# Performance work log

Hardware: AMD Instinct MI355X
Metric: run time of the kernel (lower is better)

## Reference

```python
import jax, jax.numpy as jnp
import numpy as np

D_MODEL = 1024
NUM_HEADS = 16
D_K = D_MODEL // NUM_HEADS


def setup_inputs() -> dict:
    key = jax.random.key(0)
    ks = jax.random.split(key, 8)
    s = 1.0 / np.sqrt(D_MODEL)
    inp = {
        'q': jax.random.normal(ks[0], (2, 2048, D_MODEL), jnp.float32),
        'k': jax.random.normal(ks[1], (2, 2048, D_MODEL), jnp.float32),
        'v': jax.random.normal(ks[2], (2, 2048, D_MODEL), jnp.float32),
        'Wq': jax.random.normal(ks[3], (D_MODEL, D_MODEL), jnp.float32) * s,
        'bq': jnp.zeros((D_MODEL,), jnp.float32),
        'Wk': jax.random.normal(ks[4], (D_MODEL, D_MODEL), jnp.float32) * s,
        'bk': jnp.zeros((D_MODEL,), jnp.float32),
        'Wv': jax.random.normal(ks[5], (D_MODEL, D_MODEL), jnp.float32) * s,
        'bv': jnp.zeros((D_MODEL,), jnp.float32),
        'Wo': jax.random.normal(ks[6], (D_MODEL, D_MODEL), jnp.float32) * s,
        'bo': jnp.zeros((D_MODEL,), jnp.float32),
    }
    return inp


def _split_heads(x):
    # [B, S, D] -> [B, H, S, d_k]
    b, s, _ = x.shape
    return x.reshape(b, s, NUM_HEADS, D_K).transpose(0, 2, 1, 3)


def reference(q, k, v, Wq, bq, Wk, bk, Wv, bv, Wo, bo):
    qh = _split_heads(q @ Wq + bq)
    kh = _split_heads(k @ Wk + bk)
    vh = _split_heads(v @ Wv + bv)
    scale = 1.0 / jnp.sqrt(jnp.asarray(D_K, qh.dtype))
    scores = jnp.einsum('bhqd,bhkd->bhqk', qh, kh) * scale  # [B,H,S,S]
    probs = jax.nn.softmax(scores, axis=-1)
    ctx = jnp.einsum('bhqk,bhkd->bhqd', probs, vh)
    b, h, s, d = ctx.shape
    ctx = ctx.transpose(0, 2, 1, 3).reshape(b, s, h * d)
    return ctx @ Wo + bo
```

## Files before the change

kernel.cpp:

```cpp
#include <hip/hip_runtime.h>

#define D_MODEL 1024
#define SEQ     2048
#define BATCH   2
#define NH      16
#define DK      64
#define MROWS   (BATCH*SEQ)

typedef __attribute__((ext_vector_type(8))) short short8;
typedef __attribute__((ext_vector_type(4))) float f32x4;
typedef __attribute__((ext_vector_type(16))) float f32x16;

#define QSCALE 0.18033688011112042f

#if __has_builtin(__builtin_amdgcn_exp2f)
#define EXP2(x) __builtin_amdgcn_exp2f(x)
#else
#define EXP2(x) exp2f(x)
#endif

static __device__ __forceinline__ unsigned short f2bf(float f) {
  unsigned u = __float_as_uint(f);
  u += 0x7fff + ((u >> 16) & 1);
  return (unsigned short)(u >> 16);
}

static __device__ __forceinline__ unsigned pack_bf2(float a, float b) {
  unsigned ua = __float_as_uint(a) + 0x8000u;
  unsigned ub = __float_as_uint(b) + 0x8000u;
#if __has_builtin(__builtin_amdgcn_perm)
  return __builtin_amdgcn_perm(ub, ua, 0x07060302u);
#else
  return (ua >> 16) | (ub & 0xffff0000u);
#endif
}

static __device__ __forceinline__ void plswap(unsigned& x, unsigned& y, int h) {
#if __has_builtin(__builtin_amdgcn_permlane32_swap)
  typedef __attribute__((ext_vector_type(2))) unsigned uint2v;
  uint2v r = __builtin_amdgcn_permlane32_swap(x, y, false, false);
  x = r.x; y = r.y;
#else
  unsigned xs = __shfl_xor((int)x, 32), ys = __shfl_xor((int)y, 32);
  unsigned nx = h ? ys : x;
  unsigned ny = h ? y : xs;
  x = nx; y = ny;
#endif
}

static __device__ __forceinline__ void load16_lds(const void* g, void* l) {
  __builtin_amdgcn_global_load_lds(
      (const __attribute__((address_space(1))) void*)g,
      (__attribute__((address_space(3))) void*)l, 16, 0, 0);
}

__global__ void cvt_all(const float* __restrict__ q, const float* __restrict__ k,
                        const float* __restrict__ v, unsigned short* __restrict__ out, int n4) {
  int i = blockIdx.x * blockDim.x + threadIdx.x;
  if (i >= n4) return;
  const float* src = (blockIdx.y == 0) ? q : (blockIdx.y == 1) ? k : v;
  float4 val = ((const float4*)src)[i];
  unsigned r0 = (unsigned)f2bf(val.x) | ((unsigned)f2bf(val.y) << 16);
  unsigned r1 = (unsigned)f2bf(val.z) | ((unsigned)f2bf(val.w) << 16);
  uint2 u; u.x = r0; u.y = r1;
  ((uint2*)(out + (size_t)blockIdx.y * MROWS * D_MODEL))[i] = u;
}

__global__ void wtrans_all(const float* __restrict__ Wq, const float* __restrict__ Wk,
                           const float* __restrict__ Wv, const float* __restrict__ Wo,
                           unsigned short* __restrict__ Wt) {
  __shared__ float t[32][33];
  const float* W = (blockIdx.z == 0) ? Wq : (blockIdx.z == 1) ? Wk
                 : (blockIdx.z == 2) ? Wv : Wo;
  unsigned short* dst = Wt + (size_t)blockIdx.z * D_MODEL * D_MODEL;
  int n0 = blockIdx.x * 32, k0 = blockIdx.y * 32;
  int tx = threadIdx.x & 31, ty = threadIdx.x >> 5;
#pragma unroll
  for (int i = 0; i < 32; i += 8)
    t[ty + i][tx] = W[(size_t)(k0 + ty + i) * D_MODEL + n0 + tx];
  __syncthreads();
#pragma unroll
  for (int i = 0; i < 32; i += 8)
    dst[(size_t)(n0 + ty + i) * D_MODEL + k0 + tx] = f2bf(t[tx][ty + i]);
}

__global__ __launch_bounds__(256, 2) void gemm_qkv(
    const unsigned short* __restrict__ Abig,
    const unsigned short* __restrict__ Wt,
    const float* __restrict__ bq, const float* __restrict__ bk, const float* __restrict__ bv,
    unsigned short* __restrict__ Qh, unsigned short* __restrict__ Kh,
    unsigned short* __restrict__ Vt)
{
  constexpr int K = D_MODEL;
  __shared__ unsigned short As[128 * 32];
  __shared__ unsigned short Bs[128 * 32];
  const int g = blockIdx.y >> 5;
  const unsigned short* A  = Abig + (size_t)g * MROWS * K;
  const unsigned short* Bt = Wt + (size_t)g * K * K;
  const float* bias = (g == 0) ? bq : (g == 1) ? bk : bv;
  unsigned short* out = (g == 0) ? Qh : (g == 1) ? Kh : Vt;

  const int tid  = threadIdx.x;
  const int wave = tid >> 6, lane = tid & 63;
  const int quad = lane >> 4, l16 = lane & 15;
  const int bm = (blockIdx.y & 31) * 128, bn = blockIdx.x * 128;
  const int wm = (wave >> 1) * 64, wn = (wave & 1) * 64;
  const int srow = tid >> 2, scol = (tid & 3) * 8;

  f32x4 acc[4][4] = {};
  for (int k0 = 0; k0 < K; k0 += 32) {
    load16_lds(&A [(size_t)(bm      + srow) * K + k0 + scol], &As[tid * 8]);
    load16_lds(&A [(size_t)(bm + 64 + srow) * K + k0 + scol], &As[2048 + tid * 8]);
    load16_lds(&Bt[(size_t)(bn      + srow) * K + k0 + scol], &Bs[tid * 8]);
    load16_lds(&Bt[(size_t)(bn + 64 + srow) * K + k0 + scol], &Bs[2048 + tid * 8]);
    __syncthreads();
    short8 af[4], bfr[4];
#pragma unroll
    for (int i = 0; i < 4; ++i) {
      af[i]  = *(const short8*)&As[(wm + i * 16 + l16) * 32 + quad * 8];
      bfr[i] = *(const short8*)&Bs[(wn + i * 16 + l16) * 32 + quad * 8];
    }
#pragma unroll
    for (int mt = 0; mt < 4; ++mt)
#pragma unroll
      for (int nt = 0; nt < 4; ++nt)
        acc[mt][nt] = __builtin_amdgcn_mfma_f32_16x16x32_bf16(af[mt], bfr[nt], acc[mt][nt], 0, 0, 0);
    __syncthreads();
  }

  if (g == 2) {
    float* tb = (float*)As + wave * 272;
#pragma unroll
    for (int mt = 0; mt < 4; ++mt)
#pragma unroll
      for (int nt = 0; nt < 4; ++nt) {
        int nbase = bn + wn + nt * 16;
        float bvv = bias[nbase + l16];
#pragma unroll
        for (int r = 0; r < 4; ++r)
          tb[(quad * 4 + r) * 17 + l16] = acc[mt][nt][r] + bvv;
        float v2[4];
#pragma unroll
        for (int r2 = 0; r2 < 4; ++r2)
          v2[r2] = tb[l16 * 17 + quad * 4 + r2];
        int m = bm + wm + mt * 16 + l16;
        int bb = m >> 11, s = m & 2047;
#pragma unroll
        for (int r2 = 0; r2 < 4; ++r2) {
          int n = nbase + quad * 4 + r2;
          int h = n >> 6, d = n & 63;
          out[((size_t)(bb * NH + h) * DK + d) * SEQ + s] = f2bf(v2[r2]);
        }
      }
    return;
  }

  const float scl = (g == 0) ? QSCALE : 1.0f;
#pragma unroll
  for (int mt = 0; mt < 4; ++mt)
#pragma unroll
    for (int nt = 0; nt < 4; ++nt) {
      int n = bn + wn + nt * 16 + l16;
      float bvv = bias[n];
#pragma unroll
      for (int r = 0; r < 4; ++r) {
        int m = bm + wm + mt * 16 + quad * 4 + r;
        float v = (acc[mt][nt][r] + bvv) * scl;
        int b = m >> 11, s = m & 2047;
        int h = n >> 6,  d = n & 63;
        out[((size_t)(b * NH + h) * SEQ + s) * DK + d] = f2bf(v);
      }
    }
}

__global__ __launch_bounds__(256, 2) void gemm_out(
    const unsigned short* __restrict__ A,
    const unsigned short* __restrict__ Bt,
    const float* __restrict__ bias,
    float* __restrict__ out)
{
  constexpr int K = D_MODEL;
  __shared__ unsigned short As[128 * 32];
  __shared__ unsigned short Bs[64 * 32];
  const int tid  = threadIdx.x;
  const int wave = tid >> 6, lane = tid & 63;
  const int quad = lane >> 4, l16 = lane & 15;
  const int bm = blockIdx.y * 128, bn = blockIdx.x * 64;
  const int wm = (wave >> 1) * 64, wn = (wave & 1) * 32;
  const int srow = tid >> 2, scol = (tid & 3) * 8;

  f32x4 acc[4][2] = {};
  for (int k0 = 0; k0 < K; k0 += 32) {
    load16_lds(&A [(size_t)(bm      + srow) * K + k0 + scol], &As[tid * 8]);
    load16_lds(&A [(size_t)(bm + 64 + srow) * K + k0 + scol], &As[2048 + tid * 8]);
    load16_lds(&Bt[(size_t)(bn      + srow) * K + k0 + scol], &Bs[tid * 8]);
    __syncthreads();
    short8 af[4], bfr[2];
#pragma unroll
    for (int i = 0; i < 4; ++i)
      af[i]  = *(const short8*)&As[(wm + i * 16 + l16) * 32 + quad * 8];
#pragma unroll
    for (int i = 0; i < 2; ++i)
      bfr[i] = *(const short8*)&Bs[(wn + i * 16 + l16) * 32 + quad * 8];
#pragma unroll
    for (int mt = 0; mt < 4; ++mt)
#pragma unroll
      for (int nt = 0; nt < 2; ++nt)
        acc[mt][nt] = __builtin_amdgcn_mfma_f32_16x16x32_bf16(af[mt], bfr[nt], acc[mt][nt], 0, 0, 0);
    __syncthreads();
  }
#pragma unroll
  for (int mt = 0; mt < 4; ++mt)
#pragma unroll
    for (int nt = 0; nt < 2; ++nt) {
      int n = bn + wn + nt * 16 + l16;
      float bvv = bias[n];
#pragma unroll
      for (int r = 0; r < 4; ++r) {
        int m = bm + wm + mt * 16 + quad * 4 + r;
        out[(size_t)m * D_MODEL + n] = acc[mt][nt][r] + bvv;
      }
    }
}

__global__ __launch_bounds__(512, 4) void attn(
    const unsigned short* __restrict__ Qh,
    const unsigned short* __restrict__ Kh,
    const unsigned short* __restrict__ Vt,
    unsigned short* __restrict__ ctx)
{
  const int blk = blockIdx.x;
  const int bh = blk >> 4, qt = blk & 15;
  const int tid = threadIdx.x;
  const int wave = tid >> 6, gr = wave >> 1, hk = wave & 1;
  const int lane = tid & 63, l32 = lane & 31, h = lane >> 5;
  const int srow = tid >> 3, su = tid & 7;

  __shared__ __align__(16) char smem[33280];
  unsigned short* Ks = (unsigned short*)smem;
  unsigned short* Vs = (unsigned short*)(smem + 16384);
  float* lbuf = (float*)(smem + 32768);

  const unsigned short* Kbase = Kh + (size_t)bh * SEQ * DK;
  const unsigned short* Vbase = Vt + (size_t)bh * DK * SEQ;
  const unsigned short* Qp = Qh + ((size_t)bh * SEQ + qt * 128 + gr * 32) * DK;

  short8 qf[4];
#pragma unroll
  for (int g = 0; g < 4; ++g)
    qf[g] = *(const short8*)&Qp[l32 * DK + g * 16 + h * 8];

  f32x16 cacc[2] = {};
  float lacc = 0.f;

  const int krow = hk * 32 + l32;

  short8 sk, sv;
  auto stage_load = [&](int c) {
    sk = *(const short8*)(Kbase + ((size_t)(c * 64 + srow)) * DK + su * 8);
    sv = *(const short8*)(Vbase + (size_t)srow * SEQ + c * 64 + su * 8);
  };
  auto stage_write = [&](int b) {
    int p = ((su + srow) & 7) * 8;
    *(short8*)&Ks[b * 4096 + srow * 64 + p] = sk;
    *(short8*)&Vs[b * 4096 + srow * 64 + p] = sv;
  };

  stage_load(0); stage_write(0);
  __syncthreads();

  for (int c = 0; c < SEQ / 64; ++c) {
    const int buf = c & 1;
    const bool pre = (c + 1 < SEQ / 64);
    if (pre) stage_load(c + 1);

    f32x16 s = {};
#pragma unroll
    for (int g = 0; g < 4; ++g) {
      short8 kb = *(const short8*)&Ks[buf * 4096 + krow * 64 + ((g * 2 + h + krow) & 7) * 8];
      s = __builtin_amdgcn_mfma_f32_32x32x16_bf16(kb, qf[g], s, 0, 0, 0);
    }

    float p[16];
#pragma unroll
    for (int i = 0; i < 16; ++i) p[i] = EXP2(s[i]);
    lacc += (((p[0]+p[1])+(p[2]+p[3])) + ((p[4]+p[5])+(p[6]+p[7])))
          + (((p[8]+p[9])+(p[10]+p[11])) + ((p[12]+p[13])+(p[14]+p[15])));

    unsigned pk[8];
#pragma unroll
    for (int i = 0; i < 8; ++i) pk[i] = pack_bf2(p[2 * i], p[2 * i + 1]);
    plswap(pk[0], pk[2], h); plswap(pk[1], pk[3], h);
    plswap(pk[4], pk[6], h); plswap(pk[5], pk[7], h);
    union { unsigned u[4]; short8 s8; } A0, A1;
    A0.u[0] = pk[0]; A0.u[1] = pk[1]; A0.u[2] = pk[2]; A0.u[3] = pk[3];
    A1.u[0] = pk[4]; A1.u[1] = pk[5]; A1.u[2] = pk[6]; A1.u[3] = pk[7];

#pragma unroll
    for (int nt = 0; nt < 2; ++nt) {
      int vrow = nt * 32 + l32;
      short8 vb0 = *(const short8*)&Vs[buf * 4096 + vrow * 64 + ((hk * 4 + 0 + h + vrow) & 7) * 8];
      short8 vb1 = *(const short8*)&Vs[buf * 4096 + vrow * 64 + ((hk * 4 + 2 + h + vrow) & 7) * 8];
      cacc[nt] = __builtin_amdgcn_mfma_f32_32x32x16_bf16(A0.s8, vb0, cacc[nt], 0, 0, 0);
      cacc[nt] = __builtin_amdgcn_mfma_f32_32x32x16_bf16(A1.s8, vb1, cacc[nt], 0, 0, 0);
    }

    if (pre) { stage_write(buf ^ 1); __syncthreads(); }
  }

  lacc += __shfl_xor(lacc, 32);
  __syncthreads();
  float* mb = (float*)smem + gr * 2048;
  if (hk == 1) {
#pragma unroll
    for (int nt = 0; nt < 2; ++nt)
#pragma unroll
      for (int rq = 0; rq < 4; ++rq) {
        f32x4 t;
        t[0] = cacc[nt][rq * 4 + 0]; t[1] = cacc[nt][rq * 4 + 1];
        t[2] = cacc[nt][rq * 4 + 2]; t[3] = cacc[nt][rq * 4 + 3];
        *(f32x4*)&mb[nt * 1024 + lane * 16 + rq * 4] = t;
      }
    lbuf[gr * 32 + l32] = lacc;
  }
  __syncthreads();
  if (hk == 0) {
    lacc += lbuf[gr * 32 + l32];
    float inv = 1.0f / lacc;
    float lvr[16];
#pragma unroll
    for (int r = 0; r < 16; ++r)
      lvr[r] = __shfl(inv, (r & 3) + 8 * (r >> 2) + 4 * h);
    const int b = bh >> 4, hh = bh & 15;
#pragma unroll
    for (int nt = 0; nt < 2; ++nt)
#pragma unroll
      for (int rq = 0; rq < 4; ++rq) {
        f32x4 t = *(const f32x4*)&mb[nt * 1024 + lane * 16 + rq * 4];
#pragma unroll
        for (int e = 0; e < 4; ++e) {
          int r = rq * 4 + e;
          int ql = (r & 3) + 8 * (r >> 2) + 4 * h;
          int m = qt * 128 + gr * 32 + ql;
          float val = (cacc[nt][r] + t[e]) * lvr[r];
          ctx[(size_t)(b * SEQ + m) * D_MODEL + hh * 64 + nt * 32 + l32] = f2bf(val);
        }
      }
  }
}

extern "C" void kernel_launch(void* const* d_in, const int* in_sizes, int n_in,
                              void* d_out, int out_size, void* d_ws, size_t ws_size,
                              hipStream_t stream) {
  const float* q  = (const float*)d_in[0];
  const float* k  = (const float*)d_in[1];
  const float* v  = (const float*)d_in[2];
  const float* Wq = (const float*)d_in[3];
  const float* bq = (const float*)d_in[4];
  const float* Wk = (const float*)d_in[5];
  const float* bk = (const float*)d_in[6];
  const float* Wv = (const float*)d_in[7];
  const float* bv = (const float*)d_in[8];
  const float* Wo = (const float*)d_in[9];
  const float* bo = (const float*)d_in[10];

  char* ws = (char*)d_ws;
  const size_t SZ_ACT = (size_t)MROWS * D_MODEL * 2;
  const size_t SZ_W   = (size_t)D_MODEL * D_MODEL * 2;
  unsigned short* qkvb = (unsigned short*)(ws);
  unsigned short* Wall = (unsigned short*)(ws + 3 * SZ_ACT);
  unsigned short* Qh   = (unsigned short*)(ws + 3 * SZ_ACT + 4 * SZ_W);
  unsigned short* Kh   = (unsigned short*)(ws + 4 * SZ_ACT + 4 * SZ_W);
  unsigned short* Vt   = (unsigned short*)(ws + 5 * SZ_ACT + 4 * SZ_W);
  unsigned short* Wot  = Wall + 3 * (size_t)D_MODEL * D_MODEL;
  unsigned short* ctx  = qkvb;

  int n4 = MROWS * D_MODEL / 4;
  cvt_all<<<dim3(n4 / 256, 3), 256, 0, stream>>>(q, k, v, qkvb, n4);
  wtrans_all<<<dim3(32, 32, 4), 256, 0, stream>>>(Wq, Wk, Wv, Wo, Wall);

  gemm_qkv<<<dim3(D_MODEL / 128, 96), 256, 0, stream>>>(qkvb, Wall, bq, bk, bv, Qh, Kh, Vt);

  attn<<<dim3(32 * 16), 512, 0, stream>>>(Qh, Kh, Vt, ctx);

  gemm_out<<<dim3(D_MODEL / 64, MROWS / 128), 256, 0, stream>>>(ctx, Wot, bo, (float*)d_out);
}
```

Baseline: 225.6 us.

## Merge prep kernels, double K-step in GEMMs, and widen attention KV chunks

Fuses the activation conversion and weight transpose kernels into one launch to remove a launch. Both GEMMs now load two 32-wide K slices per barrier pair, halving the number of syncs per K loop. The attention kernel stages 128 keys/values per iteration instead of 64, doubling shared memory use to cut barriers and loop overhead. The larger LDS footprint may lower occupancy.

```diff
diff --git a/kernel.cpp b/kernel.cpp
--- a/kernel.cpp
+++ b/kernel.cpp
@@ -54,26 +54,27 @@
       (__attribute__((address_space(3))) void*)l, 16, 0, 0);
 }
 
-__global__ void cvt_all(const float* __restrict__ q, const float* __restrict__ k,
-                        const float* __restrict__ v, unsigned short* __restrict__ out, int n4) {
-  int i = blockIdx.x * blockDim.x + threadIdx.x;
-  if (i >= n4) return;
-  const float* src = (blockIdx.y == 0) ? q : (blockIdx.y == 1) ? k : v;
-  float4 val = ((const float4*)src)[i];
-  unsigned r0 = (unsigned)f2bf(val.x) | ((unsigned)f2bf(val.y) << 16);
-  unsigned r1 = (unsigned)f2bf(val.z) | ((unsigned)f2bf(val.w) << 16);
-  uint2 u; u.x = r0; u.y = r1;
-  ((uint2*)(out + (size_t)blockIdx.y * MROWS * D_MODEL))[i] = u;
-}
-
-__global__ void wtrans_all(const float* __restrict__ Wq, const float* __restrict__ Wk,
-                           const float* __restrict__ Wv, const float* __restrict__ Wo,
-                           unsigned short* __restrict__ Wt) {
+__global__ void prep(const float* __restrict__ q, const float* __restrict__ k,
+                     const float* __restrict__ v,
+                     const float* __restrict__ Wq, const float* __restrict__ Wk,
+                     const float* __restrict__ Wv, const float* __restrict__ Wo,
+                     unsigned short* __restrict__ qkvb, unsigned short* __restrict__ Wall) {
   __shared__ float t[32][33];
-  const float* W = (blockIdx.z == 0) ? Wq : (blockIdx.z == 1) ? Wk
-                 : (blockIdx.z == 2) ? Wv : Wo;
-  unsigned short* dst = Wt + (size_t)blockIdx.z * D_MODEL * D_MODEL;
-  int n0 = blockIdx.x * 32, k0 = blockIdx.y * 32;
+  if (blockIdx.y < 3) {
+    int i = blockIdx.x * 256 + threadIdx.x;
+    const float* src = (blockIdx.y == 0) ? q : (blockIdx.y == 1) ? k : v;
+    float4 val = ((const float4*)src)[i];
+    unsigned r0 = (unsigned)f2bf(val.x) | ((unsigned)f2bf(val.y) << 16);
+    unsigned r1 = (unsigned)f2bf(val.z) | ((unsigned)f2bf(val.w) << 16);
+    uint2 u; u.x = r0; u.y = r1;
+    ((uint2*)(qkvb + (size_t)blockIdx.y * MROWS * D_MODEL))[i] = u;
+    return;
+  }
+  int x = blockIdx.x;
+  int w = x >> 10, rem = x & 1023;
+  int n0 = (rem >> 5) * 32, k0 = (rem & 31) * 32;
+  const float* W = (w == 0) ? Wq : (w == 1) ? Wk : (w == 2) ? Wv : Wo;
+  unsigned short* dst = Wall + (size_t)w * D_MODEL * D_MODEL;
   int tx = threadIdx.x & 31, ty = threadIdx.x >> 5;
 #pragma unroll
   for (int i = 0; i < 32; i += 8)
@@ -92,8 +93,8 @@
     unsigned short* __restrict__ Vt)
 {
   constexpr int K = D_MODEL;
-  __shared__ unsigned short As[128 * 32];
-  __shared__ unsigned short Bs[128 * 32];
+  __shared__ unsigned short As[2][128 * 32];
+  __shared__ unsigned short Bs[2][128 * 32];
   const int g = blockIdx.y >> 5;
   const unsigned short* A  = Abig + (size_t)g * MROWS * K;
   const unsigned short* Bt = Wt + (size_t)g * K * K;
@@ -108,23 +109,29 @@
   const int srow = tid >> 2, scol = (tid & 3) * 8;
 
   f32x4 acc[4][4] = {};
-  for (int k0 = 0; k0 < K; k0 += 32) {
-    load16_lds(&A [(size_t)(bm      + srow) * K + k0 + scol], &As[tid * 8]);
-    load16_lds(&A [(size_t)(bm + 64 + srow) * K + k0 + scol], &As[2048 + tid * 8]);
-    load16_lds(&Bt[(size_t)(bn      + srow) * K + k0 + scol], &Bs[tid * 8]);
-    load16_lds(&Bt[(size_t)(bn + 64 + srow) * K + k0 + scol], &Bs[2048 + tid * 8]);
+  for (int k0 = 0; k0 < K; k0 += 64) {
+#pragma unroll
+    for (int h2 = 0; h2 < 2; ++h2) {
+      load16_lds(&A [(size_t)(bm      + srow) * K + k0 + h2 * 32 + scol], &As[h2][tid * 8]);
+      load16_lds(&A [(size_t)(bm + 64 + srow) * K + k0 + h2 * 32 + scol], &As[h2][2048 + tid * 8]);
+      load16_lds(&Bt[(size_t)(bn      + srow) * K + k0 + h2 * 32 + scol], &Bs[h2][tid * 8]);
+      load16_lds(&Bt[(size_t)(bn + 64 + srow) * K + k0 + h2 * 32 + scol], &Bs[h2][2048 + tid * 8]);
+    }
     __syncthreads();
-    short8 af[4], bfr[4];
-#pragma unroll
-    for (int i = 0; i < 4; ++i) {
-      af[i]  = *(const short8*)&As[(wm + i * 16 + l16) * 32 + quad * 8];
-      bfr[i] = *(const short8*)&Bs[(wn + i * 16 + l16) * 32 + quad * 8];
-    }
-#pragma unroll
-    for (int mt = 0; mt < 4; ++mt)
-#pragma unroll
-      for (int nt = 0; nt < 4; ++nt)
-        acc[mt][nt] = __builtin_amdgcn_mfma_f32_16x16x32_bf16(af[mt], bfr[nt], acc[mt][nt], 0, 0, 0);
+#pragma unroll
+    for (int h2 = 0; h2 < 2; ++h2) {
+      short8 af[4], bfr[4];
+#pragma unroll
+      for (int i = 0; i < 4; ++i) {
+        af[i]  = *(const short8*)&As[h2][(wm + i * 16 + l16) * 32 + quad * 8];
+        bfr[i] = *(const short8*)&Bs[h2][(wn + i * 16 + l16) * 32 + quad * 8];
+      }
+#pragma unroll
+      for (int mt = 0; mt < 4; ++mt)
+#pragma unroll
+        for (int nt = 0; nt < 4; ++nt)
+          acc[mt][nt] = __builtin_amdgcn_mfma_f32_16x16x32_bf16(af[mt], bfr[nt], acc[mt][nt], 0, 0, 0);
+    }
     __syncthreads();
   }
 
@@ -148,8 +155,8 @@
 #pragma unroll
         for (int r2 = 0; r2 < 4; ++r2) {
           int n = nbase + quad * 4 + r2;
-          int h = n >> 6, d = n & 63;
-          out[((size_t)(bb * NH + h) * DK + d) * SEQ + s] = f2bf(v2[r2]);
+          int hh = n >> 6, d = n & 63;
+          out[((size_t)(bb * NH + hh) * DK + d) * SEQ + s] = f2bf(v2[r2]);
         }
       }
     return;
@@ -167,8 +174,8 @@
         int m = bm + wm + mt * 16 + quad * 4 + r;
         float v = (acc[mt][nt][r] + bvv) * scl;
         int b = m >> 11, s = m & 2047;
-        int h = n >> 6,  d = n & 63;
-        out[((size_t)(b * NH + h) * SEQ + s) * DK + d] = f2bf(v);
+        int hh = n >> 6,  d = n & 63;
+        out[((size_t)(b * NH + hh) * SEQ + s) * DK + d] = f2bf(v);
       }
     }
 }
@@ -180,8 +187,8 @@
     float* __restrict__ out)
 {
   constexpr int K = D_MODEL;
-  __shared__ unsigned short As[128 * 32];
-  __shared__ unsigned short Bs[64 * 32];
+  __shared__ unsigned short As[2][128 * 32];
+  __shared__ unsigned short Bs[2][64 * 32];
   const int tid  = threadIdx.x;
   const int wave = tid >> 6, lane = tid & 63;
   const int quad = lane >> 4, l16 = lane & 15;
@@ -190,23 +197,29 @@
   const int srow = tid >> 2, scol = (tid & 3) * 8;
 
   f32x4 acc[4][2] = {};
-  for (int k0 = 0; k0 < K; k0 += 32) {
-    load16_lds(&A [(size_t)(bm      + srow) * K + k0 + scol], &As[tid * 8]);
-    load16_lds(&A [(size_t)(bm + 64 + srow) * K + k0 + scol], &As[2048 + tid * 8]);
-    load16_lds(&Bt[(size_t)(bn      + srow) * K + k0 + scol], &Bs[tid * 8]);
+  for (int k0 = 0; k0 < K; k0 += 64) {
+#pragma unroll
+    for (int h2 = 0; h2 < 2; ++h2) {
+      load16_lds(&A [(size_t)(bm      + srow) * K + k0 + h2 * 32 + scol], &As[h2][tid * 8]);
+      load16_lds(&A [(size_t)(bm + 64 + srow) * K + k0 + h2 * 32 + scol], &As[h2][2048 + tid * 8]);
+      load16_lds(&Bt[(size_t)(bn      + srow) * K + k0 + h2 * 32 + scol], &Bs[h2][tid * 8]);
+    }
     __syncthreads();
-    short8 af[4], bfr[2];
-#pragma unroll
-    for (int i = 0; i < 4; ++i)
-      af[i]  = *(const short8*)&As[(wm + i * 16 + l16) * 32 + quad * 8];
-#pragma unroll
-    for (int i = 0; i < 2; ++i)
-      bfr[i] = *(const short8*)&Bs[(wn + i * 16 + l16) * 32 + quad * 8];
-#pragma unroll
-    for (int mt = 0; mt < 4; ++mt)
-#pragma unroll
-      for (int nt = 0; nt < 2; ++nt)
-        acc[mt][nt] = __builtin_amdgcn_mfma_f32_16x16x32_bf16(af[mt], bfr[nt], acc[mt][nt], 0, 0, 0);
+#pragma unroll
+    for (int h2 = 0; h2 < 2; ++h2) {
+      short8 af[4], bfr[2];
+#pragma unroll
+      for (int i = 0; i < 4; ++i)
+        af[i]  = *(const short8*)&As[h2][(wm + i * 16 + l16) * 32 + quad * 8];
+#pragma unroll
+      for (int i = 0; i < 2; ++i)
+        bfr[i] = *(const short8*)&Bs[h2][(wn + i * 16 + l16) * 32 + quad * 8];
+#pragma unroll
+      for (int mt = 0; mt < 4; ++mt)
+#pragma unroll
+        for (int nt = 0; nt < 2; ++nt)
+          acc[mt][nt] = __builtin_amdgcn_mfma_f32_16x16x32_bf16(af[mt], bfr[nt], acc[mt][nt], 0, 0, 0);
+    }
     __syncthreads();
   }
 #pragma unroll
@@ -234,12 +247,11 @@
   const int tid = threadIdx.x;
   const int wave = tid >> 6, gr = wave >> 1, hk = wave & 1;
   const int lane = tid & 63, l32 = lane & 31, h = lane >> 5;
-  const int srow = tid >> 3, su = tid & 7;
-
-  __shared__ __align__(16) char smem[33280];
+
+  __shared__ __align__(16) char smem[66048];
   unsigned short* Ks = (unsigned short*)smem;
-  unsigned short* Vs = (unsigned short*)(smem + 16384);
-  float* lbuf = (float*)(smem + 32768);
+  unsigned short* Vs = (unsigned short*)(smem + 32768);
+  float* lbuf = (float*)(smem + 65536);
 
   const unsigned short* Kbase = Kh + (size_t)bh * SEQ * DK;
   const unsigned short* Vbase = Vt + (size_t)bh * DK * SEQ;
@@ -253,56 +265,68 @@
   f32x16 cacc[2] = {};
   float lacc = 0.f;
 
-  const int krow = hk * 32 + l32;
-
-  short8 sk, sv;
+  const int kr0 = tid >> 3, uk = tid & 7;
+  const int vr0 = tid >> 4, uv = tid & 15;
+
+  short8 sk0, sk1, sv0, sv1;
   auto stage_load = [&](int c) {
-    sk = *(const short8*)(Kbase + ((size_t)(c * 64 + srow)) * DK + su * 8);
-    sv = *(const short8*)(Vbase + (size_t)srow * SEQ + c * 64 + su * 8);
+    const unsigned short* kg = Kbase + (size_t)(c * 128 + kr0) * DK + uk * 8;
+    sk0 = *(const short8*)kg;
+    sk1 = *(const short8*)(kg + (size_t)64 * DK);
+    const unsigned short* vg = Vbase + (size_t)vr0 * SEQ + c * 128 + uv * 8;
+    sv0 = *(const short8*)vg;
+    sv1 = *(const short8*)(vg + (size_t)32 * SEQ);
   };
   auto stage_write = [&](int b) {
-    int p = ((su + srow) & 7) * 8;
-    *(short8*)&Ks[b * 4096 + srow * 64 + p] = sk;
-    *(short8*)&Vs[b * 4096 + srow * 64 + p] = sv;
+    int pk_ = ((uk + kr0) & 7) * 8;
+    *(short8*)&Ks[b * 8192 + kr0 * 64 + pk_]        = sk0;
+    *(short8*)&Ks[b * 8192 + (kr0 + 64) * 64 + pk_] = sk1;
+    int pv_ = ((uv + vr0) & 15) * 8;
+    *(short8*)&Vs[b * 8192 + vr0 * 128 + pv_]        = sv0;
+    *(short8*)&Vs[b * 8192 + (vr0 + 32) * 128 + pv_] = sv1;
   };
 
   stage_load(0); stage_write(0);
   __syncthreads();
 
-  for (int c = 0; c < SEQ / 64; ++c) {
+  for (int c = 0; c < SEQ / 128; ++c) {
     const int buf = c & 1;
-    const bool pre = (c + 1 < SEQ / 64);
+    const bool pre = (c + 1 < SEQ / 128);
     if (pre) stage_load(c + 1);
 
-    f32x16 s = {};
-#pragma unroll
-    for (int g = 0; g < 4; ++g) {
-      short8 kb = *(const short8*)&Ks[buf * 4096 + krow * 64 + ((g * 2 + h + krow) & 7) * 8];
-      s = __builtin_amdgcn_mfma_f32_32x32x16_bf16(kb, qf[g], s, 0, 0, 0);
-    }
-
-    float p[16];
-#pragma unroll
-    for (int i = 0; i < 16; ++i) p[i] = EXP2(s[i]);
-    lacc += (((p[0]+p[1])+(p[2]+p[3])) + ((p[4]+p[5])+(p[6]+p[7])))
-          + (((p[8]+p[9])+(p[10]+p[11])) + ((p[12]+p[13])+(p[14]+p[15])));
-
-    unsigned pk[8];
-#pragma unroll
-    for (int i = 0; i < 8; ++i) pk[i] = pack_bf2(p[2 * i], p[2 * i + 1]);
-    plswap(pk[0], pk[2], h); plswap(pk[1], pk[3], h);
-    plswap(pk[4], pk[6], h); plswap(pk[5], pk[7], h);
-    union { unsigned u[4]; short8 s8; } A0, A1;
-    A0.u[0] = pk[0]; A0.u[1] = pk[1]; A0.u[2] = pk[2]; A0.u[3] = pk[3];
-    A1.u[0] = pk[4]; A1.u[1] = pk[5]; A1.u[2] = pk[6]; A1.u[3] = pk[7];
-
-#pragma unroll
-    for (int nt = 0; nt < 2; ++nt) {
-      int vrow = nt * 32 + l32;
-      short8 vb0 = *(const short8*)&Vs[buf * 4096 + vrow * 64 + ((hk * 4 + 0 + h + vrow) & 7) * 8];
-      short8 vb1 = *(const short8*)&Vs[buf * 4096 + vrow * 64 + ((hk * 4 + 2 + h + vrow) & 7) * 8];
-      cacc[nt] = __builtin_amdgcn_mfma_f32_32x32x16_bf16(A0.s8, vb0, cacc[nt], 0, 0, 0);
-      cacc[nt] = __builtin_amdgcn_mfma_f32_32x32x16_bf16(A1.s8, vb1, cacc[nt], 0, 0, 0);
+#pragma unroll
+    for (int sc = 0; sc < 2; ++sc) {
+      const int krow = sc * 64 + hk * 32 + l32;
+      f32x16 s = {};
+#pragma unroll
+      for (int g = 0; g < 4; ++g) {
+        short8 kb = *(const short8*)&Ks[buf * 8192 + krow * 64 + ((g * 2 + h + krow) & 7) * 8];
+        s = __builtin_amdgcn_mfma_f32_32x32x16_bf16(kb, qf[g], s, 0, 0, 0);
+      }
+
+      float p[16];
+#pragma unroll
+      for (int i = 0; i < 16; ++i) p[i] = EXP2(s[i]);
+      lacc += (((p[0]+p[1])+(p[2]+p[3])) + ((p[4]+p[5])+(p[6]+p[7])))
+            + (((p[8]+p[9])+(p[10]+p[11])) + ((p[12]+p[13])+(p[14]+p[15])));
+
+      unsigned pk[8];
+#pragma unroll
+      for (int i = 0; i < 8; ++i) pk[i] = pack_bf2(p[2 * i], p[2 * i + 1]);
+      plswap(pk[0], pk[2], h); plswap(pk[1], pk[3], h);
+      plswap(pk[4], pk[6], h); plswap(pk[5], pk[7], h);
+      union { unsigned u[4]; short8 s8; } A0, A1;
+      A0.u[0] = pk[0]; A0.u[1] = pk[1]; A0.u[2] = pk[2]; A0.u[3] = pk[3];
+      A1.u[0] = pk[4]; A1.u[1] = pk[5]; A1.u[2] = pk[6]; A1.u[3] = pk[7];
+
+#pragma unroll
+      for (int nt = 0; nt < 2; ++nt) {
+        int vrow = nt * 32 + l32;
+        short8 vb0 = *(const short8*)&Vs[buf * 8192 + vrow * 128 + ((sc * 8 + hk * 4 + 0 + h + vrow) & 15) * 8];
+        short8 vb1 = *(const short8*)&Vs[buf * 8192 + vrow * 128 + ((sc * 8 + hk * 4 + 2 + h + vrow) & 15) * 8];
+        cacc[nt] = __builtin_amdgcn_mfma_f32_32x32x16_bf16(A0.s8, vb0, cacc[nt], 0, 0, 0);
+        cacc[nt] = __builtin_amdgcn_mfma_f32_32x32x16_bf16(A1.s8, vb1, cacc[nt], 0, 0, 0);
+      }
     }
 
     if (pre) { stage_write(buf ^ 1); __syncthreads(); }
@@ -375,9 +399,7 @@
   unsigned short* Wot  = Wall + 3 * (size_t)D_MODEL * D_MODEL;
   unsigned short* ctx  = qkvb;
 
-  int n4 = MROWS * D_MODEL / 4;
-  cvt_all<<<dim3(n4 / 256, 3), 256, 0, stream>>>(q, k, v, qkvb, n4);
-  wtrans_all<<<dim3(32, 32, 4), 256, 0, stream>>>(Wq, Wk, Wv, Wo, Wall);
+  prep<<<dim3(4096, 4), 256, 0, stream>>>(q, k, v, Wq, Wk, Wv, Wo, qkvb, Wall);
 
   gemm_qkv<<<dim3(D_MODEL / 128, 96), 256, 0, stream>>>(qkvb, Wall, bq, bk, bv, Qh, Kh, Vt);
 
```

Result: no change. 224.2 us (-0.6%).
